# Optimization experiments

Hardware: AMD Instinct MI355X
Metric: run time of the kernel (lower is better)

Reference implementation:

```python
import jax, jax.numpy as jnp
import numpy as np

B, S, D, H = 2, 2048, 2048, 16
HD = D // H
ROPE_BASE = 10000.0
N_DOCS = 8


def setup_inputs() -> dict:
    key = jax.random.key(0)
    ks = jax.random.split(key, 7)
    scale = 1.0 / np.sqrt(D)
    x = jax.random.normal(ks[0], (B, S, D), dtype=jnp.float32)
    doc_ids = jnp.sort(jax.random.randint(ks[1], (B, S), 0, N_DOCS), axis=1)
    Wq = jax.random.normal(ks[2], (D, D), dtype=jnp.float32) * scale
    Wk = jax.random.normal(ks[3], (D, D), dtype=jnp.float32) * scale
    Wv = jax.random.normal(ks[4], (D, D), dtype=jnp.float32) * scale
    Wo = jax.random.normal(ks[5], (D, D), dtype=jnp.float32) * scale
    bo = jax.random.normal(ks[6], (D,), dtype=jnp.float32) * 0.01
    return {"x": x, "doc_ids": doc_ids, "Wq": Wq, "Wk": Wk, "Wv": Wv, "Wo": Wo, "bo": bo}


def _rotate_half(t):
    # interleaved pairs: (x0,x1,x2,x3,...) -> (-x1,x0,-x3,x2,...)
    t1 = t[..., 0::2]
    t2 = t[..., 1::2]
    return jnp.stack((-t2, t1), axis=-1).reshape(t.shape)


def _doc_position_ids(doc_ids):
    b, s = doc_ids.shape
    boundary = jnp.concatenate(
        [jnp.ones((b, 1), dtype=bool), doc_ids[:, 1:] != doc_ids[:, :-1]], axis=1)
    ar = jnp.arange(s)[None, :]
    boundary_pos = jnp.where(boundary, ar, 0)
    last_boundary = jax.lax.cummax(boundary_pos, axis=1)
    return ar - last_boundary  # position within each document


def reference(x, doc_ids, Wq, Wk, Wv, Wo, bo):
    b, s, d = x.shape
    h, hd = H, HD

    q = (x @ Wq).reshape(b, s, h, hd).transpose(0, 2, 1, 3)  # [b,h,s,hd]
    k = (x @ Wk).reshape(b, s, h, hd).transpose(0, 2, 1, 3)
    v = (x @ Wv).reshape(b, s, h, hd).transpose(0, 2, 1, 3)

    # doc-aware RoPE: positions reset at document boundaries
    pos = _doc_position_ids(doc_ids).astype(jnp.float32)  # [b,s]
    inv_freq = 1.0 / (ROPE_BASE ** (jnp.arange(0, hd, 2, dtype=jnp.float32) / hd))
    freqs = pos[..., None] * inv_freq  # [b,s,hd/2]
    cos = jnp.repeat(jnp.cos(freqs), 2, axis=-1)[:, None]  # [b,1,s,hd]
    sin = jnp.repeat(jnp.sin(freqs), 2, axis=-1)[:, None]
    q = q * cos + _rotate_half(q) * sin
    k = k * cos + _rotate_half(k) * sin

    scores = jnp.einsum("bhqd,bhkd->bhqk", q, k)
    # doc-blockwise causal mask: attend only to j<=i within same document
    same_doc = doc_ids[:, :, None] == doc_ids[:, None, :]  # [b,s,s] (i,j)
    allowed = jnp.tril(same_doc)[:, None]  # [b,1,s,s]
    inv_scale = 1.0 / np.sqrt(hd)
    scores = jnp.where(allowed, scores * inv_scale, -jnp.inf)
    attn = jax.nn.softmax(scores, axis=-1)

    ctx = jnp.einsum("bhqk,bhkd->bhqd", attn, v)
    ctx = ctx.transpose(0, 2, 1, 3).reshape(b, s, d)
    return ctx @ Wo + bo
```

## Files before the change

kernel.cpp:

```cpp
#include <hip/hip_runtime.h>
#include <hip/hip_bf16.h>

#define Dd 2048
#define Ss 2048
#define Bb 2
#define Hh 16
#define HDd 128
#define BSs (Bb*Ss)
#define NTIL 32

typedef __bf16 bf16;
typedef __bf16 bf16x8 __attribute__((ext_vector_type(8)));
typedef __bf16 bf16x4 __attribute__((ext_vector_type(4)));
typedef float f32x4 __attribute__((ext_vector_type(4)));

__device__ __forceinline__ void gload_lds16(const void* g, void* l) {
  __builtin_amdgcn_global_load_lds((__attribute__((address_space(1))) void*)(g),
                                   (__attribute__((address_space(3))) void*)(l), 16, 0, 0);
}

template <int N>
__device__ __forceinline__ void waitv() {
  if constexpr (N == 0) asm volatile("s_waitcnt vmcnt(0)" ::: "memory");
  else if constexpr (N == 6) asm volatile("s_waitcnt vmcnt(6)" ::: "memory");
}

__global__ void k_prep(const float* __restrict__ x, bf16* __restrict__ xb,
                       const float* __restrict__ Wq, const float* __restrict__ Wk,
                       const float* __restrict__ Wv, const float* __restrict__ Wo,
                       bf16* __restrict__ wqkvt, bf16* __restrict__ wot) {
  __shared__ float t[64][65];
  int zz = blockIdx.z;
  int tid = threadIdx.x;

  if (zz == 4) {
    int id = blockIdx.y * 32 + blockIdx.x;
    size_t base = (size_t)id * 8192 + tid * 4;
#pragma unroll
    for (int it = 0; it < 8; it++) {
      size_t i = base + (size_t)it * 1024;
      f32x4 v = *(const f32x4*)(x + i);
      bf16x4 o;
      o[0] = (bf16)v[0]; o[1] = (bf16)v[1]; o[2] = (bf16)v[2]; o[3] = (bf16)v[3];
      *(bf16x4*)(xb + i) = o;
    }
    return;
  }

  const float* W = (zz == 0) ? Wq : (zz == 1) ? Wk : (zz == 2) ? Wv : Wo;
  bf16* T = (zz < 3) ? (wqkvt + (size_t)zz * Dd * Dd) : wot;
  int n0 = blockIdx.x * 64, k0 = blockIdx.y * 64;
#pragma unroll
  for (int rr = 0; rr < 4; rr++) {
    int r = (tid >> 4) + rr * 16;
    f32x4 vv = *(const f32x4*)(W + (size_t)(k0 + r) * Dd + n0 + (tid & 15) * 4);
#pragma unroll
    for (int j = 0; j < 4; j++) t[r][(tid & 15) * 4 + j] = vv[j];
  }
  __syncthreads();
#pragma unroll
  for (int rr = 0; rr < 4; rr++) {
    int n = rr * 16 + (tid >> 4);
    int kb = (tid & 15) * 4;
    bf16x4 o;
#pragma unroll
    for (int j = 0; j < 4; j++) o[j] = (bf16)t[kb + j][n];
    *(bf16x4*)(T + (size_t)(n0 + n) * Dd + k0 + kb) = o;
  }
}

__global__ void k_pos(const int* __restrict__ doc, int* __restrict__ pos) {
  int b = blockIdx.x;
  __shared__ int bp[2][Ss];
  const int* db = doc + (size_t)b * Ss;
  for (int i = threadIdx.x; i < Ss; i += 1024) {
    int bd = (i == 0) || (db[i] != db[i - 1]);
    bp[0][i] = bd ? i : 0;
  }
  __syncthreads();
  int src = 0;
  for (int off = 1; off < Ss; off <<= 1) {
    for (int i = threadIdx.x; i < Ss; i += 1024) {
      int v = bp[src][i];
      if (i >= off) v = max(v, bp[src][i - off]);
      bp[1 - src][i] = v;
    }
    __syncthreads();
    src = 1 - src;
  }
  for (int i = threadIdx.x; i < Ss; i += 1024)
    pos[(size_t)b * Ss + i] = i - bp[src][i];
}

__device__ __forceinline__ void stage64(const char* gA, const char* gB,
                                        int m0, int n0, int t, int buf,
                                        char* AL, char* BL, int tid) {
  int ktb = t * 128;
#pragma unroll
  for (int p = 0; p < 2; p++) {
    int o = p * 8192 + tid * 16;
    int r = o >> 7, cb = o & 127;
    gload_lds16(gA + (size_t)(m0 + r) * 4096 + ktb + (cb ^ ((r & 7) << 4)),
                AL + buf * 16384 + o);
  }
#pragma unroll
  for (int p = 0; p < 4; p++) {
    int o = p * 8192 + tid * 16;
    int r = o >> 7, cb = o & 127;
    gload_lds16(gB + (size_t)(n0 + r) * 4096 + ktb + (cb ^ ((r & 7) << 4)),
                BL + buf * 32768 + o);
  }
}

template <bool STAGE, int WV>
__device__ __forceinline__ void do_tile64(const char* gA, const char* gB, int m0, int n0,
                                          int t, int bi, int b2, char* AL, char* BL, int tid,
                                          int wr, int wc, int ln, int g,
                                          f32x4 (&acc)[4][4]) {
  if (STAGE) stage64(gA, gB, m0, n0, t + 2, b2, AL, BL, tid);
  const char* tA = AL + bi * 16384;
  const char* tB = BL + bi * 32768;
#pragma unroll
  for (int kk = 0; kk < 2; kk++) {
    bf16x8 af[4], bf[4];
#pragma unroll
    for (int mq = 0; mq < 4; mq++) {
      int row = wr * 64 + mq * 16 + ln;
      af[mq] = *(const bf16x8*)(tA + row * 128 + ((kk * 64 + g * 16) ^ ((row & 7) << 4)));
    }
#pragma unroll
    for (int nq = 0; nq < 4; nq++) {
      int row = wc * 64 + nq * 16 + ln;
      bf[nq] = *(const bf16x8*)(tB + row * 128 + ((kk * 64 + g * 16) ^ ((row & 7) << 4)));
    }
    __builtin_amdgcn_s_setprio(1);
#pragma unroll
    for (int mq = 0; mq < 4; mq++)
#pragma unroll
      for (int nq = 0; nq < 4; nq++)
        acc[mq][nq] = __builtin_amdgcn_mfma_f32_16x16x32_bf16(af[mq], bf[nq], acc[mq][nq], 0, 0, 0);
    __builtin_amdgcn_s_setprio(0);
  }
  waitv<WV>();
  __builtin_amdgcn_s_barrier();
}

__device__ __forceinline__ void gemm64_core(const bf16* gA_, const bf16* gB_,
                                            int m0, int n0, char* AL, char* BL,
                                            f32x4 (&acc)[4][4]) {
  const char* gA = (const char*)gA_;
  const char* gB = (const char*)gB_;
  const int tid = threadIdx.x;
  const int l = tid & 63, w = tid >> 6;
  const int wr = w >> 2, wc = w & 3;
  const int g = l >> 4, ln = l & 15;
  f32x4 z = {0.f, 0.f, 0.f, 0.f};
#pragma unroll
  for (int i = 0; i < 4; i++)
#pragma unroll
    for (int n = 0; n < 4; n++) acc[i][n] = z;

  stage64(gA, gB, m0, n0, 0, 0, AL, BL, tid);
  stage64(gA, gB, m0, n0, 1, 1, AL, BL, tid);
  waitv<6>();
  __builtin_amdgcn_s_barrier();

  for (int tt = 0; tt < 10; tt++) {
    int t = tt * 3;
    do_tile64<true, 6>(gA, gB, m0, n0, t,     0, 2, AL, BL, tid, wr, wc, ln, g, acc);
    do_tile64<true, 6>(gA, gB, m0, n0, t + 1, 1, 0, AL, BL, tid, wr, wc, ln, g, acc);
    do_tile64<true, 6>(gA, gB, m0, n0, t + 2, 2, 1, AL, BL, tid, wr, wc, ln, g, acc);
  }
  do_tile64<false, 0>(gA, gB, m0, n0, 30, 0, 0, AL, BL, tid, wr, wc, ln, g, acc);
  do_tile64<false, -1>(gA, gB, m0, n0, 31, 1, 0, AL, BL, tid, wr, wc, ln, g, acc);
}

__global__ __launch_bounds__(512, 2) void k_qkv256(const bf16* __restrict__ xb,
                                                   const bf16* __restrict__ wqkvt,
                                                   const int* __restrict__ pos,
                                                   bf16* __restrict__ q,
                                                   bf16* __restrict__ k,
                                                   bf16* __restrict__ vt) {
  __shared__ char SLM[147456];
  char* AL = SLM;
  char* BL = SLM + 49152;
  int bid = blockIdx.x;
  int x = bid & 7, j = bid >> 3;
  int mt = j / 3, nt = x * 3 + (j % 3);
  int m0 = mt * 128, n0 = nt * 256;

  f32x4 acc[4][4];
  gemm64_core(xb, wqkvt, m0, n0, AL, BL, acc);

  const int tid = threadIdx.x;
  const int l = tid & 63, w = tid >> 6;
  const int wr = w >> 2, wc = w & 3, g = l >> 4, ln = l & 15;
  int z = n0 >> 11;
  int n0l = n0 & 2047;
  int bix = m0 >> 11;
  int sl0 = m0 & 2047;

  if (z == 2) {
#pragma unroll
    for (int mq = 0; mq < 4; mq++) {
      int sl = sl0 + wr * 64 + mq * 16 + g * 4;
#pragma unroll
      for (int nq = 0; nq < 4; nq++) {
        int col = n0l + wc * 64 + nq * 16 + ln;
        int h = col >> 7, hd = col & 127;
        bf16x4 o;
#pragma unroll
        for (int r2 = 0; r2 < 4; r2++) o[r2] = (bf16)acc[mq][nq][r2];
        *(bf16x4*)(vt + (((size_t)(bix * Hh + h) * HDd + hd) * Ss + sl)) = o;
      }
    }
  } else {
    bf16* dst = (z == 0) ? q : k;
    float* T = (float*)SLM;
    const float c1 = 0.14391156642398168f;
    int cg = (tid & 31) * 8;
    int hb = n0l + cg;
    int hh = hb >> 7, hd0 = hb & 127;
    float fr[4];
#pragma unroll
    for (int pr = 0; pr < 4; pr++)
      fr[pr] = __expf(-(float)((hd0 >> 1) + pr) * c1);

#pragma unroll
    for (int pass = 0; pass < 2; pass++) {
      __syncthreads();
      if (wr == pass) {
#pragma unroll
        for (int mq = 0; mq < 4; mq++) {
#pragma unroll
          for (int nq = 0; nq < 4; nq++) {
            int c = wc * 64 + nq * 16 + ln;
            int rb = mq * 16 + g * 4;
#pragma unroll
            for (int r2 = 0; r2 < 4; r2++)
              T[(rb + r2) * 260 + c] = acc[mq][nq][r2];
          }
        }
      }
      __syncthreads();
#pragma unroll
      for (int j2 = 0; j2 < 4; j2++) {
        int r = j2 * 16 + (tid >> 5);
        int sg = m0 + pass * 64 + r;
        float p = (float)pos[sg];
        f32x4 v0 = *(const f32x4*)(T + r * 260 + cg);
        f32x4 v1 = *(const f32x4*)(T + r * 260 + cg + 4);
        float e0[4] = {v0[0], v0[2], v1[0], v1[2]};
        float e1[4] = {v0[1], v0[3], v1[1], v1[3]};
        int s = sg & 2047;
        bf16x8 o;
#pragma unroll
        for (int pr = 0; pr < 4; pr++) {
          float ang = p * fr[pr];
          float sn, cs;
          __sincosf(ang, &sn, &cs);
          o[2 * pr]     = (bf16)(e0[pr] * cs - e1[pr] * sn);
          o[2 * pr + 1] = (bf16)(e1[pr] * cs + e0[pr] * sn);
        }
        *(bf16x8*)(dst + (((size_t)(bix * Hh + hh) * Ss + s) * HDd + hd0)) = o;
      }
    }
  }
}

__global__ __launch_bounds__(512, 2) void k_out256(const bf16* __restrict__ ctx,
                                                   const bf16* __restrict__ wot,
                                                   const float* __restrict__ bo,
                                                   float* __restrict__ outp) {
  __shared__ char AL[49152];
  __shared__ char BL[98304];
  int bid = blockIdx.x;
  int x = bid & 7, j = bid >> 3;
  int mt = j, nt = x;
  int m0 = mt * 128, n0 = nt * 256;

  f32x4 acc[4][4];
  gemm64_core(ctx, wot, m0, n0, AL, BL, acc);

  const int l = threadIdx.x & 63, w = threadIdx.x >> 6;
  const int wr = w >> 2, wc = w & 3, g = l >> 4, ln = l & 15;
  float bov[4];
#pragma unroll
  for (int nq = 0; nq < 4; nq++)
    bov[nq] = bo[n0 + wc * 64 + nq * 16 + ln];
#pragma unroll
  for (int mq = 0; mq < 4; mq++)
#pragma unroll
    for (int r2 = 0; r2 < 4; r2++) {
      int row = m0 + wr * 64 + mq * 16 + g * 4 + r2;
#pragma unroll
      for (int nq = 0; nq < 4; nq++) {
        int col = n0 + wc * 64 + nq * 16 + ln;
        outp[(size_t)row * Dd + col] = acc[mq][nq][r2] + bov[nq];
      }
    }
}

__global__ __launch_bounds__(256) void k_attn(const bf16* __restrict__ q,
                                              const bf16* __restrict__ k,
                                              const bf16* __restrict__ vt,
                                              const int* __restrict__ pos,
                                              bf16* __restrict__ ctx) {
  __shared__ bf16 Ks[64 * 128];
  __shared__ bf16 Vts[128 * 64];
  __shared__ bf16 Pw[4][16 * 64];
  int bid = blockIdx.x;
  int xc = bid & 7, jj = bid >> 3;
  int bh = xc * 4 + (jj >> 5);
  int qt = jj & 31;
  int b = bh >> 4, h = bh & 15;
  int q0 = qt * 64;
  const int tid = threadIdx.x, l = tid & 63, w = tid >> 6, g = l >> 4, ln = l & 15;
  const bf16* qb = q + (size_t)bh * Ss * HDd;
  const bf16* kb = k + (size_t)bh * Ss * HDd;
  const bf16* vb = vt + (size_t)bh * Ss * HDd;

  bf16x8 qf[4];
  int qr = q0 + w * 16 + ln;
#pragma unroll
  for (int ks = 0; ks < 4; ks++)
    qf[ks] = *(const bf16x8*)(qb + (size_t)qr * HDd + ks * 32 + 8 * g);

  int rrow[4], dstart[4];
  float m[4], lsum[4];
#pragma unroll
  for (int r2 = 0; r2 < 4; r2++) {
    rrow[r2] = q0 + w * 16 + 4 * g + r2;
    dstart[r2] = rrow[r2] - pos[(size_t)b * Ss + rrow[r2]];
    m[r2] = -1e30f;
    lsum[r2] = 0.f;
  }
  f32x4 oacc[8];
  f32x4 z = {0.f, 0.f, 0.f, 0.f};
#pragma unroll
  for (int n = 0; n < 8; n++) oacc[n] = z;

  int kt_start = (q0 - pos[(size_t)b * Ss + q0]) >> 6;
  const float iscale = 0.08838834764831845f;

  for (int kt = kt_start; kt <= qt; kt++) {
    int kv0 = kt * 64;
#pragma unroll
    for (int i2 = 0; i2 < 4; i2++) {
      int o = i2 * 4096 + w * 1024 + l * 16;
      int rk = o >> 8, cbk = o & 255;
      gload_lds16((const char*)kb + (size_t)(kv0 + rk) * 256 + cbk,
                  (char*)Ks + i2 * 4096 + w * 1024);
      int rv = o >> 7, cbv = o & 127;
      gload_lds16((const char*)vb + (size_t)rv * (Ss * 2) + (size_t)kv0 * 2 + cbv,
                  (char*)Vts + i2 * 4096 + w * 1024);
    }
    __syncthreads();

    f32x4 sc[4];
#pragma unroll
    for (int n = 0; n < 4; n++) {
      f32x4 a = z;
#pragma unroll
      for (int ks = 0; ks < 4; ks++) {
        bf16x8 bfrag = *(const bf16x8*)(Ks + (n * 16 + ln) * 128 + ks * 32 + 8 * g);
        a = __builtin_amdgcn_mfma_f32_16x16x32_bf16(qf[ks], bfrag, a, 0, 0, 0);
      }
      sc[n] = a;
    }

    float pmax[4] = {-1e30f, -1e30f, -1e30f, -1e30f};
    float pv[4][4];
#pragma unroll
    for (int n = 0; n < 4; n++) {
      int kvc = kv0 + n * 16 + ln;
#pragma unroll
      for (int r2 = 0; r2 < 4; r2++) {
        bool ok = (kvc <= rrow[r2]) && (kvc >= dstart[r2]);
        float sv = ok ? sc[n][r2] * iscale : -1e30f;
        pv[n][r2] = sv;
        pmax[r2] = fmaxf(pmax[r2], sv);
      }
    }
#pragma unroll
    for (int off = 1; off < 16; off <<= 1)
#pragma unroll
      for (int r2 = 0; r2 < 4; r2++)
        pmax[r2] = fmaxf(pmax[r2], __shfl_xor(pmax[r2], off, 64));

    float alpha[4];
#pragma unroll
    for (int r2 = 0; r2 < 4; r2++) {
      float mn = fmaxf(m[r2], pmax[r2]);
      alpha[r2] = __expf(m[r2] - mn);
      m[r2] = mn;
    }

    float rs[4] = {0.f, 0.f, 0.f, 0.f};
#pragma unroll
    for (int n = 0; n < 4; n++) {
      int kvc = kv0 + n * 16 + ln;
#pragma unroll
      for (int r2 = 0; r2 < 4; r2++) {
        bool ok = (kvc <= rrow[r2]) && (kvc >= dstart[r2]);
        float p = ok ? __expf(pv[n][r2] - m[r2]) : 0.f;
        rs[r2] += p;
        Pw[w][(4 * g + r2) * 64 + n * 16 + ln] = (bf16)p;
      }
    }
#pragma unroll
    for (int off = 1; off < 16; off <<= 1)
#pragma unroll
      for (int r2 = 0; r2 < 4; r2++) rs[r2] += __shfl_xor(rs[r2], off, 64);
#pragma unroll
    for (int r2 = 0; r2 < 4; r2++) lsum[r2] = lsum[r2] * alpha[r2] + rs[r2];
#pragma unroll
    for (int n = 0; n < 8; n++)
#pragma unroll
      for (int r2 = 0; r2 < 4; r2++) oacc[n][r2] *= alpha[r2];
    __syncthreads();

#pragma unroll
    for (int n = 0; n < 8; n++) {
#pragma unroll
      for (int ks = 0; ks < 2; ks++) {
        bf16x8 pa = *(const bf16x8*)(&Pw[w][ln * 64 + ks * 32 + 8 * g]);
        bf16x8 vfr = *(const bf16x8*)(Vts + (n * 16 + ln) * 64 + ks * 32 + 8 * g);
        oacc[n] = __builtin_amdgcn_mfma_f32_16x16x32_bf16(pa, vfr, oacc[n], 0, 0, 0);
      }
    }
    __syncthreads();
  }

#pragma unroll
  for (int n = 0; n < 8; n++)
#pragma unroll
    for (int r2 = 0; r2 < 4; r2++) {
      float val = oacc[n][r2] / lsum[r2];
      ctx[((size_t)(b * Ss + rrow[r2])) * Dd + h * HDd + n * 16 + ln] = (bf16)val;
    }
}

extern "C" void kernel_launch(void* const* d_in, const int* in_sizes, int n_in,
                              void* d_out, int out_size, void* d_ws, size_t ws_size,
                              hipStream_t stream) {
  const float* x = (const float*)d_in[0];
  const int* doc = (const int*)d_in[1];
  const float* Wq = (const float*)d_in[2];
  const float* Wk = (const float*)d_in[3];
  const float* Wv = (const float*)d_in[4];
  const float* Wo = (const float*)d_in[5];
  const float* bo = (const float*)d_in[6];
  float* outp = (float*)d_out;

  char* ws = (char*)d_ws;
  size_t off = 0;
  auto alloc = [&](size_t bytes) {
    char* p = ws + off;
    off += (bytes + 255) & ~(size_t)255;
    return p;
  };
  bf16* xb = (bf16*)alloc((size_t)BSs * Dd * 2);
  bf16* wqkvt = (bf16*)alloc((size_t)3 * Dd * Dd * 2);
  bf16* wot = (bf16*)alloc((size_t)Dd * Dd * 2);
  bf16* qd = (bf16*)alloc((size_t)BSs * Dd * 2);
  bf16* kd = (bf16*)alloc((size_t)BSs * Dd * 2);
  bf16* vtd = (bf16*)alloc((size_t)BSs * Dd * 2);
  bf16* ctxd = (bf16*)alloc((size_t)BSs * Dd * 2);
  int* pos = (int*)alloc((size_t)BSs * 4);

  k_prep<<<dim3(Dd / 64, Dd / 64, 5), 256, 0, stream>>>(x, xb, Wq, Wk, Wv, Wo, wqkvt, wot);
  k_pos<<<Bb, 1024, 0, stream>>>(doc, pos);
  k_qkv256<<<dim3(768), 512, 0, stream>>>(xb, wqkvt, pos, qd, kd, vtd);
  k_attn<<<dim3(1024), 256, 0, stream>>>(qd, kd, vtd, pos, ctxd);
  k_out256<<<dim3(256), 512, 0, stream>>>(ctxd, wot, bo, outp);
}
```

Measured before the change: 218.5 us.

## Fuse pos scan into prep, loop QKV tiles per block, balance attention tiles

The doc-position scan is folded into the prep kernel as an extra z-slice, which drops one kernel launch. The QKV GEMM now launches 256 blocks, each looping over three N tiles instead of 768 single-tile blocks, so one wave fits on the CUs and the block tail shrinks. The attention grid interleaves short and long causal query tiles so per-block work evens out. The risks are less latency hiding in the QKV kernel, and most z=5 prep blocks are launched only to exit immediately.

```diff
diff --git a/kernel.cpp b/kernel.cpp
--- a/kernel.cpp
+++ b/kernel.cpp
@@ -28,8 +28,9 @@
 __global__ void k_prep(const float* __restrict__ x, bf16* __restrict__ xb,
                        const float* __restrict__ Wq, const float* __restrict__ Wk,
                        const float* __restrict__ Wv, const float* __restrict__ Wo,
-                       bf16* __restrict__ wqkvt, bf16* __restrict__ wot) {
-  __shared__ float t[64][65];
+                       bf16* __restrict__ wqkvt, bf16* __restrict__ wot,
+                       const int* __restrict__ doc, int* __restrict__ pos) {
+  __shared__ char smem[16640];
   int zz = blockIdx.z;
   int tid = threadIdx.x;
 
@@ -47,6 +48,32 @@
     return;
   }
 
+  if (zz == 5) {
+    if (blockIdx.x >= Bb || blockIdx.y != 0) return;
+    int b = blockIdx.x;
+    int* bp = (int*)smem;
+    const int* db = doc + (size_t)b * Ss;
+    for (int i = tid; i < Ss; i += 256) {
+      int bd = (i == 0) || (db[i] != db[i - 1]);
+      bp[i] = bd ? i : 0;
+    }
+    __syncthreads();
+    int src = 0;
+    for (int off = 1; off < Ss; off <<= 1) {
+      for (int i = tid; i < Ss; i += 256) {
+        int v = bp[src * Ss + i];
+        if (i >= off) v = max(v, bp[src * Ss + i - off]);
+        bp[(1 - src) * Ss + i] = v;
+      }
+      __syncthreads();
+      src = 1 - src;
+    }
+    for (int i = tid; i < Ss; i += 256)
+      pos[(size_t)b * Ss + i] = i - bp[src * Ss + i];
+    return;
+  }
+
+  float (*t)[65] = (float(*)[65])smem;
   const float* W = (zz == 0) ? Wq : (zz == 1) ? Wk : (zz == 2) ? Wv : Wo;
   bf16* T = (zz < 3) ? (wqkvt + (size_t)zz * Dd * Dd) : wot;
   int n0 = blockIdx.x * 64, k0 = blockIdx.y * 64;
@@ -67,29 +94,6 @@
     for (int j = 0; j < 4; j++) o[j] = (bf16)t[kb + j][n];
     *(bf16x4*)(T + (size_t)(n0 + n) * Dd + k0 + kb) = o;
   }
-}
-
-__global__ void k_pos(const int* __restrict__ doc, int* __restrict__ pos) {
-  int b = blockIdx.x;
-  __shared__ int bp[2][Ss];
-  const int* db = doc + (size_t)b * Ss;
-  for (int i = threadIdx.x; i < Ss; i += 1024) {
-    int bd = (i == 0) || (db[i] != db[i - 1]);
-    bp[0][i] = bd ? i : 0;
-  }
-  __syncthreads();
-  int src = 0;
-  for (int off = 1; off < Ss; off <<= 1) {
-    for (int i = threadIdx.x; i < Ss; i += 1024) {
-      int v = bp[src][i];
-      if (i >= off) v = max(v, bp[src][i - off]);
-      bp[1 - src][i] = v;
-    }
-    __syncthreads();
-    src = 1 - src;
-  }
-  for (int i = threadIdx.x; i < Ss; i += 1024)
-    pos[(size_t)b * Ss + i] = i - bp[src][i];
 }
 
 __device__ __forceinline__ void stage64(const char* gA, const char* gB,
@@ -185,86 +189,92 @@
   char* AL = SLM;
   char* BL = SLM + 49152;
   int bid = blockIdx.x;
-  int x = bid & 7, j = bid >> 3;
-  int mt = j / 3, nt = x * 3 + (j % 3);
-  int m0 = mt * 128, n0 = nt * 256;
-
-  f32x4 acc[4][4];
-  gemm64_core(xb, wqkvt, m0, n0, AL, BL, acc);
+  int x = bid & 7, mt = bid >> 3;
+  int m0 = mt * 128;
 
   const int tid = threadIdx.x;
   const int l = tid & 63, w = tid >> 6;
   const int wr = w >> 2, wc = w & 3, g = l >> 4, ln = l & 15;
-  int z = n0 >> 11;
-  int n0l = n0 & 2047;
   int bix = m0 >> 11;
   int sl0 = m0 & 2047;
 
-  if (z == 2) {
-#pragma unroll
-    for (int mq = 0; mq < 4; mq++) {
-      int sl = sl0 + wr * 64 + mq * 16 + g * 4;
-#pragma unroll
-      for (int nq = 0; nq < 4; nq++) {
-        int col = n0l + wc * 64 + nq * 16 + ln;
-        int h = col >> 7, hd = col & 127;
-        bf16x4 o;
-#pragma unroll
-        for (int r2 = 0; r2 < 4; r2++) o[r2] = (bf16)acc[mq][nq][r2];
-        *(bf16x4*)(vt + (((size_t)(bix * Hh + h) * HDd + hd) * Ss + sl)) = o;
-      }
-    }
-  } else {
-    bf16* dst = (z == 0) ? q : k;
-    float* T = (float*)SLM;
-    const float c1 = 0.14391156642398168f;
-    int cg = (tid & 31) * 8;
-    int hb = n0l + cg;
-    int hh = hb >> 7, hd0 = hb & 127;
-    float fr[4];
-#pragma unroll
-    for (int pr = 0; pr < 4; pr++)
-      fr[pr] = __expf(-(float)((hd0 >> 1) + pr) * c1);
-
-#pragma unroll
-    for (int pass = 0; pass < 2; pass++) {
-      __syncthreads();
-      if (wr == pass) {
-#pragma unroll
-        for (int mq = 0; mq < 4; mq++) {
-#pragma unroll
-          for (int nq = 0; nq < 4; nq++) {
-            int c = wc * 64 + nq * 16 + ln;
-            int rb = mq * 16 + g * 4;
-#pragma unroll
-            for (int r2 = 0; r2 < 4; r2++)
-              T[(rb + r2) * 260 + c] = acc[mq][nq][r2];
+#pragma unroll 1
+  for (int ni = 0; ni < 3; ni++) {
+    int nt = x * 3 + ni;
+    int n0 = nt * 256;
+    f32x4 acc[4][4];
+    gemm64_core(xb, wqkvt, m0, n0, AL, BL, acc);
+
+    int z = n0 >> 11;
+    int n0l = n0 & 2047;
+
+    if (z == 2) {
+#pragma unroll
+      for (int mq = 0; mq < 4; mq++) {
+        int sl = sl0 + wr * 64 + mq * 16 + g * 4;
+#pragma unroll
+        for (int nq = 0; nq < 4; nq++) {
+          int col = n0l + wc * 64 + nq * 16 + ln;
+          int h = col >> 7, hd = col & 127;
+          bf16x4 o;
+#pragma unroll
+          for (int r2 = 0; r2 < 4; r2++) o[r2] = (bf16)acc[mq][nq][r2];
+          *(bf16x4*)(vt + (((size_t)(bix * Hh + h) * HDd + hd) * Ss + sl)) = o;
+        }
+      }
+    } else {
+      bf16* dst = (z == 0) ? q : k;
+      float* T = (float*)SLM;
+      const float c1 = 0.14391156642398168f;
+      int cg = (tid & 31) * 8;
+      int hb = n0l + cg;
+      int hh = hb >> 7, hd0 = hb & 127;
+      float fr[4];
+#pragma unroll
+      for (int pr = 0; pr < 4; pr++)
+        fr[pr] = __expf(-(float)((hd0 >> 1) + pr) * c1);
+
+#pragma unroll
+      for (int pass = 0; pass < 2; pass++) {
+        __syncthreads();
+        if (wr == pass) {
+#pragma unroll
+          for (int mq = 0; mq < 4; mq++) {
+#pragma unroll
+            for (int nq = 0; nq < 4; nq++) {
+              int c = wc * 64 + nq * 16 + ln;
+              int rb = mq * 16 + g * 4;
+#pragma unroll
+              for (int r2 = 0; r2 < 4; r2++)
+                T[(rb + r2) * 260 + c] = acc[mq][nq][r2];
+            }
           }
         }
-      }
-      __syncthreads();
-#pragma unroll
-      for (int j2 = 0; j2 < 4; j2++) {
-        int r = j2 * 16 + (tid >> 5);
-        int sg = m0 + pass * 64 + r;
-        float p = (float)pos[sg];
-        f32x4 v0 = *(const f32x4*)(T + r * 260 + cg);
-        f32x4 v1 = *(const f32x4*)(T + r * 260 + cg + 4);
-        float e0[4] = {v0[0], v0[2], v1[0], v1[2]};
-        float e1[4] = {v0[1], v0[3], v1[1], v1[3]};
-        int s = sg & 2047;
-        bf16x8 o;
-#pragma unroll
-        for (int pr = 0; pr < 4; pr++) {
-          float ang = p * fr[pr];
-          float sn, cs;
-          __sincosf(ang, &sn, &cs);
-          o[2 * pr]     = (bf16)(e0[pr] * cs - e1[pr] * sn);
-          o[2 * pr + 1] = (bf16)(e1[pr] * cs + e0[pr] * sn);
+        __syncthreads();
+#pragma unroll
+        for (int j2 = 0; j2 < 4; j2++) {
+          int r = j2 * 16 + (tid >> 5);
+          int sg = m0 + pass * 64 + r;
+          float p = (float)pos[sg];
+          f32x4 v0 = *(const f32x4*)(T + r * 260 + cg);
+          f32x4 v1 = *(const f32x4*)(T + r * 260 + cg + 4);
+          float e0[4] = {v0[0], v0[2], v1[0], v1[2]};
+          float e1[4] = {v0[1], v0[3], v1[1], v1[3]};
+          int s = sg & 2047;
+          bf16x8 o;
+#pragma unroll
+          for (int pr = 0; pr < 4; pr++) {
+            float ang = p * fr[pr];
+            float sn, cs;
+            __sincosf(ang, &sn, &cs);
+            o[2 * pr]     = (bf16)(e0[pr] * cs - e1[pr] * sn);
+            o[2 * pr + 1] = (bf16)(e1[pr] * cs + e0[pr] * sn);
+          }
+          *(bf16x8*)(dst + (((size_t)(bix * Hh + hh) * Ss + s) * HDd + hd0)) = o;
         }
-        *(bf16x8*)(dst + (((size_t)(bix * Hh + hh) * Ss + s) * HDd + hd0)) = o;
-      }
-    }
+      }
+    }
+    __syncthreads();
   }
 }
 
@@ -312,7 +322,8 @@
   int bid = blockIdx.x;
   int xc = bid & 7, jj = bid >> 3;
   int bh = xc * 4 + (jj >> 5);
-  int qt = jj & 31;
+  int idx5 = jj & 31;
+  int qt = (idx5 & 1) ? (31 - (idx5 >> 1)) : (idx5 >> 1);
   int b = bh >> 4, h = bh & 15;
   int q0 = qt * 64;
   const int tid = threadIdx.x, l = tid & 63, w = tid >> 6, g = l >> 4, ln = l & 15;
@@ -469,9 +480,8 @@
   bf16* ctxd = (bf16*)alloc((size_t)BSs * Dd * 2);
   int* pos = (int*)alloc((size_t)BSs * 4);
 
-  k_prep<<<dim3(Dd / 64, Dd / 64, 5), 256, 0, stream>>>(x, xb, Wq, Wk, Wv, Wo, wqkvt, wot);
-  k_pos<<<Bb, 1024, 0, stream>>>(doc, pos);
-  k_qkv256<<<dim3(768), 512, 0, stream>>>(xb, wqkvt, pos, qd, kd, vtd);
+  k_prep<<<dim3(32, 32, 6), 256, 0, stream>>>(x, xb, Wq, Wk, Wv, Wo, wqkvt, wot, doc, pos);
+  k_qkv256<<<dim3(256), 512, 0, stream>>>(xb, wqkvt, pos, qd, kd, vtd);
   k_attn<<<dim3(1024), 256, 0, stream>>>(qd, kd, vtd, pos, ctxd);
   k_out256<<<dim3(256), 512, 0, stream>>>(ctxd, wot, bo, outp);
 }
```

New measurement: 216.3 us. Within noise of the previous version (-1.0%).
